# Kernel tuning notes

Measured on AMD Instinct MI355X. Metric: run time of the kernel, lower is better.

Reference implementation:

```python
import jax, jax.numpy as jnp
import numpy as np

D_MODEL = 1024
D_INNER = 2048  # d_model * expand_factor
EPS = 1e-6


def setup_inputs() -> dict:
    key = jax.random.key(0)
    ks = jax.random.split(key, 9)
    s_in = 1.0 / np.sqrt(D_MODEL)
    s_out = 1.0 / np.sqrt(D_INNER)
    x = jax.random.normal(ks[0], (4, 2048, D_MODEL), dtype=jnp.float32)
    # weights stored as [in, out] (transpose of nn.Linear layout)
    Wq = jax.random.uniform(ks[1], (D_MODEL, D_INNER), jnp.float32, -s_in, s_in)
    bq = jax.random.uniform(ks[2], (D_INNER,), jnp.float32, -s_in, s_in)
    Wk = jax.random.uniform(ks[3], (D_MODEL, D_INNER), jnp.float32, -s_in, s_in)
    bk = jax.random.uniform(ks[4], (D_INNER,), jnp.float32, -s_in, s_in)
    Wv = jax.random.uniform(ks[5], (D_MODEL, D_INNER), jnp.float32, -s_in, s_in)
    bv = jax.random.uniform(ks[6], (D_INNER,), jnp.float32, -s_in, s_in)
    Wo = jax.random.uniform(ks[7], (D_INNER, D_MODEL), jnp.float32, -s_out, s_out)
    bo = jax.random.uniform(ks[8], (D_MODEL,), jnp.float32, -s_out, s_out)
    return {"x": x, "Wq": Wq, "bq": bq, "Wk": Wk, "bk": bk,
            "Wv": Wv, "bv": bv, "Wo": Wo, "bo": bo}


def _phi(x):
    """ELU + 1 feature map (positive features)."""
    return jax.nn.elu(x) + 1.0


def reference(x, Wq, bq, Wk, bk, Wv, bv, Wo, bo):
    # x: [B, N, d_model]
    Q = _phi(x @ Wq + bq)          # [B, N, d_inner]
    K = _phi(x @ Wk + bk)          # [B, N, d_inner]
    V = x @ Wv + bv                # [B, N, d_inner]
    n = x.shape[1]
    # Causal linear attention; identical math to cumsum-of-outer-products:
    # numerator_n = sum_{m<=n} (Q_n . K_m) V_m ; denominator_n = sum_{m<=n} Q_n . K_m
    scores = jnp.einsum("bnd,bmd->bnm", Q, K)            # [B, N, N]
    mask = jnp.tril(jnp.ones((n, n), dtype=scores.dtype))
    scores = scores * mask
    numerator = jnp.einsum("bnm,bme->bne", scores, V)    # [B, N, d_inner]
    denominator = scores.sum(axis=-1, keepdims=True) + EPS
    out = numerator / denominator
    return out @ Wo + bo           # [B, N, d_model] (dropout is identity in eval)
```

## Files before the change

### kernel.cpp

```cpp
#include <hip/hip_runtime.h>
#include <hip/hip_bf16.h>


#define D_MODEL 1024
#define D_INNER 2048
#define SEQ     2048
#define NBATCH  4
#define MTOT    (NBATCH * SEQ)

typedef __attribute__((ext_vector_type(8))) __bf16 bf16x8;
typedef __attribute__((ext_vector_type(4))) float  f32x4;
typedef __attribute__((ext_vector_type(8))) short  short8v;
typedef __attribute__((ext_vector_type(4))) int    int4v;
typedef __attribute__((ext_vector_type(8))) int    int8v;

__device__ __forceinline__ short f2bf(float f) {
  union { float f; unsigned u; } x; x.f = f;
  unsigned r = x.u + 0x7fffu + ((x.u >> 16) & 1u);
  return (short)(r >> 16);
}
__device__ __forceinline__ float bf2f(short s) {
  union { unsigned u; float f; } x; x.u = ((unsigned)(unsigned short)s) << 16;
  return x.f;
}

__device__ __forceinline__ unsigned char f2fp8(float f) {
  union { float f; unsigned u; } x; x.f = f;
  const unsigned s = (x.u >> 24) & 0x80u;
  const unsigned a = x.u & 0x7fffffffu;
  if (a >= 0x43E00000u) return (unsigned char)(s | 0x7Eu);
  if (a < 0x3C800000u) {
    union { float f; unsigned u; } y; y.u = a;
    const int mi = (int)rintf(y.f * 512.0f);
    return (unsigned char)(s | (unsigned)mi);
  }
  const unsigned r = a + 0x7FFFFu + ((a >> 20) & 1u);
  const unsigned E = (r >> 23) - 120u;
  return (unsigned char)(s | (E << 3) | ((r >> 20) & 7u));
}

typedef const void __attribute__((address_space(1)))* as1cv;
typedef void __attribute__((address_space(3)))* as3v;

__device__ __forceinline__ void gload_lds16(const void* g, void* l) {
  __builtin_amdgcn_global_load_lds((as1cv)g, (as3v)l, 16, 0, 0);
}

__device__ __forceinline__ f32x4 mfma16(bf16x8 a, bf16x8 b, f32x4 c) {
  return __builtin_amdgcn_mfma_f32_16x16x32_bf16(a, b, c, 0, 0, 0);
}

__device__ __forceinline__ f32x4 mfma_fp8(int8v a, int8v b, f32x4 c) {
  asm("v_mfma_f32_16x16x128_f8f6f4 %0, %1, %2, %0"
      : "+v"(c) : "v"(a), "v"(b));
  return c;
}

__device__ __forceinline__ void gemm_pipe(const short* __restrict__ A, int lda, int aRowBase,
                                          const short* __restrict__ B, int ldb, int bRowBase,
                                          int k0, int k1, short* smem, f32x4 acc[4][4]) {
  const int t    = threadIdx.x;
  const int lane = t & 63, wid = t >> 6;
  const int wr = wid >> 1, wc = wid & 1;
  const int lrow = lane & 15, kblk = lane >> 4;

  const int r0 = t >> 2;
  const int sc = ((t & 3) ^ ((t >> 3) & 3)) * 8;
  const short* pA = A + (size_t)(aRowBase + r0) * lda + (k0 + sc);
  const short* pB = B + (size_t)(bRowBase + r0) * ldb + (k0 + sc);
  const size_t rA = (size_t)64 * lda;
  const size_t rB = (size_t)64 * ldb;

  int aoff[4], boff[4];
#pragma unroll
  for (int m = 0; m < 4; ++m) {
    const int row = wr * 64 + m * 16 + lrow;
    aoff[m] = (row * 64 + kblk * 16) ^ (((row >> 1) & 3) << 4);
  }
#pragma unroll
  for (int n = 0; n < 4; ++n) {
    const int row = wc * 64 + n * 16 + lrow;
    boff[n] = (row * 64 + kblk * 16) ^ (((row >> 1) & 3) << 4);
  }
  const char* cs = (const char*)smem;

#define STG(bufShorts) do {                                                    \
    gload_lds16(pA, smem + (bufShorts) + t * 8);                               \
    gload_lds16(pA + rA, smem + (bufShorts) + 2048 + t * 8);                   \
    gload_lds16(pB, smem + (bufShorts) + 4096 + t * 8);                        \
    gload_lds16(pB + rB, smem + (bufShorts) + 6144 + t * 8);                   \
    pA += 32; pB += 32;                                                        \
  } while (0)

#define CSTEP(bufBytes) do {                                                   \
    bf16x8 a[4], b[4];                                                         \
    _Pragma("unroll") for (int m = 0; m < 4; ++m)                              \
      a[m] = *(const bf16x8*)(cs + (bufBytes) + aoff[m]);                      \
    _Pragma("unroll") for (int n = 0; n < 4; ++n)                              \
      b[n] = *(const bf16x8*)(cs + (bufBytes) + 8192 + boff[n]);               \
    _Pragma("unroll") for (int m = 0; m < 4; ++m)                              \
      _Pragma("unroll") for (int n = 0; n < 4; ++n)                            \
        acc[m][n] = mfma16(a[m], b[n], acc[m][n]);                             \
  } while (0)

  STG(0);
  __syncthreads();
  for (int k = k0; k < k1; k += 64) {
    if (k + 32 < k1) STG(8192);
    CSTEP(0);
    __syncthreads();
    if (k + 64 < k1) STG(0);
    CSTEP(16384);
    __syncthreads();
  }
#undef STG
#undef CSTEP
}

__device__ __forceinline__ void gemm_pipe8(const unsigned char* __restrict__ A, int lda, int aRowBase,
                                           const unsigned char* __restrict__ B, int ldb, int bRowBase,
                                           int k0, int k1, char* smem, f32x4 acc[4][4]) {
  const int t    = threadIdx.x;
  const int lane = t & 63, wid = t >> 6;
  const int wr = wid >> 1, wc = wid & 1;
  const int lrow = lane & 15, kblk = lane >> 4;

  const int srow = t >> 3;
  const int scol = (((t & 7) ^ ((t >> 3) & 7)) << 4);
  const unsigned char* pA = A + (size_t)(aRowBase + srow) * lda + (k0 + scol);
  const unsigned char* pB = B + (size_t)(bRowBase + srow) * ldb + (k0 + scol);

  int aoff[4][2], boff[4][2];
#pragma unroll
  for (int m = 0; m < 4; ++m) {
    const int row = wr * 64 + m * 16 + lrow;
#pragma unroll
    for (int j = 0; j < 2; ++j)
      aoff[m][j] = row * 128 + (((kblk * 2 + j) ^ (row & 7)) << 4);
  }
#pragma unroll
  for (int n = 0; n < 4; ++n) {
    const int row = wc * 64 + n * 16 + lrow;
#pragma unroll
    for (int j = 0; j < 2; ++j)
      boff[n][j] = row * 128 + (((kblk * 2 + j) ^ (row & 7)) << 4);
  }

#define STG8(bufB) do {                                                        \
    _Pragma("unroll") for (int i = 0; i < 4; ++i) {                            \
      gload_lds16(pA + (size_t)(32 * i) * lda, smem + (bufB) + i * 4096 + t * 16);      \
      gload_lds16(pB + (size_t)(32 * i) * ldb, smem + (bufB) + 16384 + i * 4096 + t * 16); \
    }                                                                          \
    pA += 128; pB += 128;                                                      \
  } while (0)

#define CSTEP8(bufB) do {                                                      \
    int8v a[4], b[4];                                                          \
    _Pragma("unroll") for (int m = 0; m < 4; ++m)                              \
      _Pragma("unroll") for (int j = 0; j < 2; ++j)                            \
        ((int4v*)&a[m])[j] = *(const int4v*)(smem + (bufB) + aoff[m][j]);      \
    _Pragma("unroll") for (int n = 0; n < 4; ++n)                              \
      _Pragma("unroll") for (int j = 0; j < 2; ++j)                            \
        ((int4v*)&b[n])[j] = *(const int4v*)(smem + (bufB) + 16384 + boff[n][j]); \
    _Pragma("unroll") for (int m = 0; m < 4; ++m)                              \
      _Pragma("unroll") for (int n = 0; n < 4; ++n)                            \
        acc[m][n] = mfma_fp8(a[m], b[n], acc[m][n]);                           \
  } while (0)

  STG8(0);
  __syncthreads();
  for (int k = k0; k < k1; k += 256) {
    if (k + 128 < k1) STG8(32768);
    CSTEP8(0);
    __syncthreads();
    if (k + 256 < k1) STG8(0);
    CSTEP8(32768);
    __syncthreads();
  }
#undef STG8
#undef CSTEP8
}

#define GEMM_PRE                                           \
  __shared__ __align__(16) short smem[4 * 4096];           \
  f32x4 acc[4][4];                                         \
  _Pragma("unroll")                                        \
  for (int m = 0; m < 4; ++m)                              \
    _Pragma("unroll")                                      \
    for (int n = 0; n < 4; ++n) acc[m][n] = (f32x4){0.f, 0.f, 0.f, 0.f};

#define GEMM_PRE8                                          \
  __shared__ __align__(16) char smem8[65536];              \
  f32x4 acc[4][4];                                         \
  _Pragma("unroll")                                        \
  for (int m = 0; m < 4; ++m)                              \
    _Pragma("unroll")                                      \
    for (int n = 0; n < 4; ++n) acc[m][n] = (f32x4){0.f, 0.f, 0.f, 0.f};

#define EPILOG_VARS                                        \
  const int lane = threadIdx.x & 63;                       \
  const int wid  = threadIdx.x >> 6;                       \
  const int wr = wid >> 1, wc = wid & 1;                   \
  const int lrow = lane & 15, kblk = lane >> 4;

__global__ __launch_bounds__(256) void k_proj_qk8(const unsigned char* __restrict__ X8,
                                                  const unsigned char* __restrict__ WT8,
                                                  const float* __restrict__ bq,
                                                  const float* __restrict__ bk,
                                                  unsigned char* __restrict__ Qm8,
                                                  unsigned char* __restrict__ Km8) {
  GEMM_PRE8
  const int blockM = blockIdx.y * 128;
  const int blockN = blockIdx.x * 128;
  gemm_pipe8(X8, D_MODEL, blockM, WT8, D_MODEL, blockN, 0, D_MODEL, smem8, acc);
  EPILOG_VARS
  const int seg = blockN >> 11;
  const float* bias = (seg == 0) ? bq : bk;
  unsigned char* dst = (seg == 0) ? Qm8 : Km8;
#pragma unroll
  for (int m = 0; m < 4; ++m)
#pragma unroll
    for (int n = 0; n < 4; ++n) {
      const int e = (blockN & 2047) + wc * 64 + n * 16 + lrow;
      const float bvv = bias[e];
#pragma unroll
      for (int j = 0; j < 4; ++j) {
        const int row = blockM + wr * 64 + m * 16 + kblk * 4 + j;
        float v = acc[m][n][j] + bvv;
        v = (v > 0.f) ? (v + 1.f) : __expf(v);
        dst[(size_t)row * D_INNER + e] = f2fp8(v);
      }
    }
}

__global__ __launch_bounds__(256) void k_proj_v(const short* __restrict__ X,
                                                const short* __restrict__ WvT,
                                                const float* __restrict__ bv,
                                                short* __restrict__ vT) {
  GEMM_PRE
  const int blockM = blockIdx.y * 128;
  const int blockN = blockIdx.x * 128;
  gemm_pipe(X, D_MODEL, blockM, WvT, D_MODEL, blockN, 0, D_MODEL, smem, acc);
  EPILOG_VARS
#pragma unroll
  for (int m = 0; m < 4; ++m)
#pragma unroll
    for (int n = 0; n < 4; ++n) {
      const int cl = wc * 64 + n * 16 + lrow;
      const float bvv = bv[blockN + cl];
#pragma unroll
      for (int j = 0; j < 4; ++j) {
        const int rl = wr * 64 + m * 16 + kblk * 4 + j;
        int byte = cl * 256 + rl * 2;
        byte ^= (cl & 7) << 5;
        *(short*)((char*)smem + byte) = f2bf(acc[m][n][j] + bvv);
      }
    }
  __syncthreads();
  const int b   = blockM >> 11;
  const int mm0 = blockM & 2047;
  const int er  = threadIdx.x >> 1;
  const int hf  = threadIdx.x & 1;
  short* dst = vT + ((size_t)b * D_INNER + blockN + er) * SEQ + mm0 + hf * 64;
#pragma unroll
  for (int i = 0; i < 8; ++i) {
    int byte = er * 256 + hf * 128 + i * 16;
    byte ^= (er & 7) << 5;
    ((short8v*)dst)[i] = *(const short8v*)((const char*)smem + byte);
  }
}

__global__ __launch_bounds__(256) void k_qkt8(const unsigned char* __restrict__ Q8,
                                              const unsigned char* __restrict__ K8,
                                              short* __restrict__ S,
                                              float* __restrict__ den_part) {
  const int b = blockIdx.y;
  const int t = blockIdx.x;
  int ib = (int)((-1.0f + sqrtf(8.0f * (float)t + 1.0f)) * 0.5f);
  while ((ib + 1) * (ib + 2) / 2 <= t) ++ib;
  while (ib * (ib + 1) / 2 > t) --ib;
  const int jb = t - ib * (ib + 1) / 2;
  GEMM_PRE8
  short* Sb = S + (size_t)b * SEQ * SEQ;
  gemm_pipe8(Q8 + (size_t)b * SEQ * D_INNER, D_INNER, ib * 128,
             K8 + (size_t)b * SEQ * D_INNER, D_INNER, jb * 128,
             0, D_INNER, smem8, acc);
  EPILOG_VARS
  const bool diag = (jb == ib);
  float sums[4][4];
#pragma unroll
  for (int m = 0; m < 4; ++m)
#pragma unroll
    for (int j = 0; j < 4; ++j) sums[m][j] = 0.f;
#pragma unroll
  for (int m = 0; m < 4; ++m)
#pragma unroll
    for (int n = 0; n < 4; ++n) {
      const int col = jb * 128 + wc * 64 + n * 16 + lrow;
#pragma unroll
      for (int j = 0; j < 4; ++j) {
        const int row = ib * 128 + wr * 64 + m * 16 + kblk * 4 + j;
        float v = acc[m][n][j];
        if (diag && col > row) v = 0.f;
        const short bs = f2bf(v);
        Sb[(size_t)row * SEQ + col] = bs;
        sums[m][j] += bf2f(bs);
      }
    }
#pragma unroll
  for (int m = 0; m < 4; ++m)
#pragma unroll
    for (int j = 0; j < 4; ++j) {
      float red = sums[m][j];
      red += __shfl_xor(red, 1, 64);
      red += __shfl_xor(red, 2, 64);
      red += __shfl_xor(red, 4, 64);
      red += __shfl_xor(red, 8, 64);
      if (lrow == 0) {
        const int rloc = wr * 64 + m * 16 + kblk * 4 + j;
        den_part[(size_t)(2 * jb + wc) * MTOT + b * SEQ + ib * 128 + rloc] = red;
      }
    }
}

__global__ __launch_bounds__(256) void k_av(const short* __restrict__ S,
                                            const short* __restrict__ VT,
                                            const float* __restrict__ den_part,
                                            short* __restrict__ attn) {
  const int b = blockIdx.z;
  const int ib = 15 - blockIdx.y;
  const int eb = blockIdx.x;
  __shared__ float dnm[128];
  {
    const int t = threadIdx.x;
    if (t < 128) {
      float s = 1e-6f;
      const int nv = 2 * (ib + 1);
      const float* dp = den_part + b * SEQ + ib * 128 + t;
      for (int q = 0; q < nv; ++q) s += dp[(size_t)q * MTOT];
      dnm[t] = 1.0f / s;
    }
  }
  GEMM_PRE
  gemm_pipe(S + (size_t)b * SEQ * SEQ, SEQ, ib * 128,
            VT + (size_t)b * (size_t)D_INNER * SEQ, SEQ, eb * 128,
            0, (ib + 1) * 128, smem, acc);
  EPILOG_VARS
  const int blockM = ib * 128;
#pragma unroll
  for (int m = 0; m < 4; ++m)
#pragma unroll
    for (int j = 0; j < 4; ++j) {
      const int rloc = wr * 64 + m * 16 + kblk * 4 + j;
      const int row = blockM + rloc;
      const float rcp = dnm[rloc];
#pragma unroll
      for (int n = 0; n < 4; ++n) {
        const int col = eb * 128 + wc * 64 + n * 16 + lrow;
        attn[((size_t)(b * SEQ + row)) * D_INNER + col] = f2bf(acc[m][n][j] * rcp);
      }
    }
}

__global__ __launch_bounds__(256) void k_out(const short* __restrict__ A,
                                             const short* __restrict__ WoT,
                                             const float* __restrict__ bo,
                                             float* __restrict__ out) {
  GEMM_PRE
  const int blockM = blockIdx.y * 128;
  const int blockN = blockIdx.x * 128;
  gemm_pipe(A, D_INNER, blockM, WoT, D_INNER, blockN, 0, D_INNER, smem, acc);
  EPILOG_VARS
#pragma unroll
  for (int m = 0; m < 4; ++m)
#pragma unroll
    for (int n = 0; n < 4; ++n) {
      const int col = blockN + wc * 64 + n * 16 + lrow;
      const float bvv = bo[col];
#pragma unroll
      for (int j = 0; j < 4; ++j) {
        const int row = blockM + wr * 64 + m * 16 + kblk * 4 + j;
        out[(size_t)row * D_MODEL + col] = acc[m][n][j] + bvv;
      }
    }
}

__global__ void k_cvt(const float* __restrict__ in, short* __restrict__ outb,
                      unsigned char* __restrict__ out8, int n4) {
  int i = blockIdx.x * blockDim.x + threadIdx.x;
  const int stride = gridDim.x * blockDim.x;
  for (; i < n4; i += stride) {
    float4 v = ((const float4*)in)[i];
    short4 o;
    o.x = f2bf(v.x); o.y = f2bf(v.y); o.z = f2bf(v.z); o.w = f2bf(v.w);
    ((short4*)outb)[i] = o;
    uchar4 q;
    q.x = f2fp8(v.x); q.y = f2fp8(v.y); q.z = f2fp8(v.z); q.w = f2fp8(v.w);
    ((uchar4*)out8)[i] = q;
  }
}

__global__ __launch_bounds__(256) void k_transposeAll(const float* __restrict__ w0,
                                                      const float* __restrict__ w1,
                                                      const float* __restrict__ w2,
                                                      const float* __restrict__ w3,
                                                      unsigned char* __restrict__ wqkT8,
                                                      short* __restrict__ wvT,
                                                      short* __restrict__ woT) {
  __shared__ float tl[32][33];
  const int z = blockIdx.z;
  const float* in = (z == 0) ? w0 : (z == 1) ? w1 : (z == 2) ? w2 : w3;
  const int R = (z < 3) ? 1024 : 2048;
  const int C = (z < 3) ? 2048 : 1024;
  const int nbx = C >> 5;
  const int c0 = (blockIdx.x % nbx) * 32, r0 = (blockIdx.x / nbx) * 32;
  const int tx = threadIdx.x & 31, ty = (threadIdx.x >> 5) * 4;
#pragma unroll
  for (int i = 0; i < 4; ++i)
    tl[ty + i][tx] = in[(size_t)(r0 + ty + i) * C + (c0 + tx)];
  __syncthreads();
  if (z < 2) {
    unsigned char* o = wqkT8 + (size_t)z * D_INNER * D_MODEL;
#pragma unroll
    for (int i = 0; i < 4; ++i)
      o[(size_t)(c0 + ty + i) * R + (r0 + tx)] = f2fp8(tl[tx][ty + i]);
  } else {
    short* o = (z == 2) ? wvT : woT;
#pragma unroll
    for (int i = 0; i < 4; ++i)
      o[(size_t)(c0 + ty + i) * R + (r0 + tx)] = f2bf(tl[tx][ty + i]);
  }
}

extern "C" void kernel_launch(void* const* d_in, const int* in_sizes, int n_in,
                              void* d_out, int out_size, void* d_ws, size_t ws_size,
                              hipStream_t stream) {
  const float* x  = (const float*)d_in[0];
  const float* Wq = (const float*)d_in[1];
  const float* bq = (const float*)d_in[2];
  const float* Wk = (const float*)d_in[3];
  const float* bk = (const float*)d_in[4];
  const float* Wv = (const float*)d_in[5];
  const float* bv = (const float*)d_in[6];
  const float* Wo = (const float*)d_in[7];
  const float* bo = (const float*)d_in[8];
  float* out = (float*)d_out;

  short* xb    = (short*)d_ws;
  short* wvT   = xb    + (size_t)MTOT * D_MODEL;
  short* woT   = wvT   + (size_t)D_INNER * D_MODEL;
  short* vT    = woT   + (size_t)D_MODEL * D_INNER;
  short* Sc    = vT    + (size_t)MTOT * D_INNER;
  short* attn  = Sc    + (size_t)NBATCH * SEQ * SEQ;
  unsigned char* x8    = (unsigned char*)(attn + (size_t)MTOT * D_INNER);
  unsigned char* wqkT8 = x8    + (size_t)MTOT * D_MODEL;
  unsigned char* Qm8   = wqkT8 + (size_t)2 * D_INNER * D_MODEL;
  unsigned char* Km8   = Qm8   + (size_t)MTOT * D_INNER;
  float* den_part      = (float*)(Km8 + (size_t)MTOT * D_INNER);

  dim3 b256(256);
  k_cvt<<<2048, b256, 0, stream>>>(x, xb, x8, MTOT * D_MODEL / 4);
  k_transposeAll<<<dim3(2048, 1, 4), b256, 0, stream>>>(Wq, Wk, Wv, Wo, wqkT8, wvT, woT);

  k_proj_qk8<<<dim3(32, 64), b256, 0, stream>>>(x8, wqkT8, bq, bk, Qm8, Km8);
  k_proj_v  <<<dim3(16, 64), b256, 0, stream>>>(xb, wvT, bv, vT);

  k_qkt8<<<dim3(136, NBATCH), b256, 0, stream>>>(Qm8, Km8, Sc, den_part);
  k_av  <<<dim3(16, 16, NBATCH), b256, 0, stream>>>(Sc, vT, den_part, attn);
  k_out <<<dim3(8, 64), b256, 0, stream>>>(attn, woT, bo, out);
}
```

Measured before the change: 303.8 us.

## Reassociate attention output as S·(V·Wo) to shrink the causal GEMM width

Computes V·Wo first into a per-batch transposed buffer, then multiplies the causal score matrix by this narrower product and applies the normalization and output bias in the epilogue. This halves the N dimension of the triangular score-value GEMM and removes the separate attention-output intermediate and final projection kernel. The trade-off is an extra rounding to bf16 of V·Wo before the causal sum, which may change numerical error.

Result: faster. 284.5 us (-6.3%).

```diff
diff --git a/kernel.cpp b/kernel.cpp
--- a/kernel.cpp
+++ b/kernel.cpp
@@ -236,7 +236,7 @@
 __global__ __launch_bounds__(256) void k_proj_v(const short* __restrict__ X,
                                                 const short* __restrict__ WvT,
                                                 const float* __restrict__ bv,
-                                                short* __restrict__ vT) {
+                                                short* __restrict__ V) {
   GEMM_PRE
   const int blockM = blockIdx.y * 128;
   const int blockN = blockIdx.x * 128;
@@ -246,14 +246,35 @@
   for (int m = 0; m < 4; ++m)
 #pragma unroll
     for (int n = 0; n < 4; ++n) {
+      const int e = blockN + wc * 64 + n * 16 + lrow;
+      const float bvv = bv[e];
+#pragma unroll
+      for (int j = 0; j < 4; ++j) {
+        const int row = blockM + wr * 64 + m * 16 + kblk * 4 + j;
+        V[(size_t)row * D_INNER + e] = f2bf(acc[m][n][j] + bvv);
+      }
+    }
+}
+
+__global__ __launch_bounds__(256) void k_vw(const short* __restrict__ V,
+                                            const short* __restrict__ WoT,
+                                            short* __restrict__ w2T) {
+  GEMM_PRE
+  const int blockM = blockIdx.y * 128;
+  const int blockN = blockIdx.x * 128;
+  gemm_pipe(V, D_INNER, blockM, WoT, D_INNER, blockN, 0, D_INNER, smem, acc);
+  EPILOG_VARS
+#pragma unroll
+  for (int m = 0; m < 4; ++m)
+#pragma unroll
+    for (int n = 0; n < 4; ++n) {
       const int cl = wc * 64 + n * 16 + lrow;
-      const float bvv = bv[blockN + cl];
 #pragma unroll
       for (int j = 0; j < 4; ++j) {
         const int rl = wr * 64 + m * 16 + kblk * 4 + j;
         int byte = cl * 256 + rl * 2;
         byte ^= (cl & 7) << 5;
-        *(short*)((char*)smem + byte) = f2bf(acc[m][n][j] + bvv);
+        *(short*)((char*)smem + byte) = f2bf(acc[m][n][j]);
       }
     }
   __syncthreads();
@@ -261,7 +282,7 @@
   const int mm0 = blockM & 2047;
   const int er  = threadIdx.x >> 1;
   const int hf  = threadIdx.x & 1;
-  short* dst = vT + ((size_t)b * D_INNER + blockN + er) * SEQ + mm0 + hf * 64;
+  short* dst = w2T + ((size_t)b * D_MODEL + blockN + er) * SEQ + mm0 + hf * 64;
 #pragma unroll
   for (int i = 0; i < 8; ++i) {
     int byte = er * 256 + hf * 128 + i * 16;
@@ -323,10 +344,11 @@
     }
 }
 
-__global__ __launch_bounds__(256) void k_av(const short* __restrict__ S,
-                                            const short* __restrict__ VT,
+__global__ __launch_bounds__(256) void k_sv(const short* __restrict__ S,
+                                            const short* __restrict__ W2T,
                                             const float* __restrict__ den_part,
-                                            short* __restrict__ attn) {
+                                            const float* __restrict__ bo,
+                                            float* __restrict__ out) {
   const int b = blockIdx.z;
   const int ib = 15 - blockIdx.y;
   const int eb = blockIdx.x;
@@ -343,7 +365,7 @@
   }
   GEMM_PRE
   gemm_pipe(S + (size_t)b * SEQ * SEQ, SEQ, ib * 128,
-            VT + (size_t)b * (size_t)D_INNER * SEQ, SEQ, eb * 128,
+            W2T + (size_t)b * (size_t)D_MODEL * SEQ, SEQ, eb * 128,
             0, (ib + 1) * 128, smem, acc);
   EPILOG_VARS
   const int blockM = ib * 128;
@@ -357,30 +379,7 @@
 #pragma unroll
       for (int n = 0; n < 4; ++n) {
         const int col = eb * 128 + wc * 64 + n * 16 + lrow;
-        attn[((size_t)(b * SEQ + row)) * D_INNER + col] = f2bf(acc[m][n][j] * rcp);
-      }
-    }
-}
-
-__global__ __launch_bounds__(256) void k_out(const short* __restrict__ A,
-                                             const short* __restrict__ WoT,
-                                             const float* __restrict__ bo,
-                                             float* __restrict__ out) {
-  GEMM_PRE
-  const int blockM = blockIdx.y * 128;
-  const int blockN = blockIdx.x * 128;
-  gemm_pipe(A, D_INNER, blockM, WoT, D_INNER, blockN, 0, D_INNER, smem, acc);
-  EPILOG_VARS
-#pragma unroll
-  for (int m = 0; m < 4; ++m)
-#pragma unroll
-    for (int n = 0; n < 4; ++n) {
-      const int col = blockN + wc * 64 + n * 16 + lrow;
-      const float bvv = bo[col];
-#pragma unroll
-      for (int j = 0; j < 4; ++j) {
-        const int row = blockM + wr * 64 + m * 16 + kblk * 4 + j;
-        out[(size_t)row * D_MODEL + col] = acc[m][n][j] + bvv;
+        out[((size_t)(b * SEQ + row)) * D_MODEL + col] = acc[m][n][j] * rcp + bo[col];
       }
     }
 }
@@ -449,10 +448,10 @@
   short* xb    = (short*)d_ws;
   short* wvT   = xb    + (size_t)MTOT * D_MODEL;
   short* woT   = wvT   + (size_t)D_INNER * D_MODEL;
-  short* vT    = woT   + (size_t)D_MODEL * D_INNER;
-  short* Sc    = vT    + (size_t)MTOT * D_INNER;
-  short* attn  = Sc    + (size_t)NBATCH * SEQ * SEQ;
-  unsigned char* x8    = (unsigned char*)(attn + (size_t)MTOT * D_INNER);
+  short* V     = woT   + (size_t)D_MODEL * D_INNER;
+  short* Sc    = V     + (size_t)MTOT * D_INNER;
+  short* w2T   = Sc    + (size_t)NBATCH * SEQ * SEQ;
+  unsigned char* x8    = (unsigned char*)(w2T + (size_t)NBATCH * D_MODEL * SEQ);
   unsigned char* wqkT8 = x8    + (size_t)MTOT * D_MODEL;
   unsigned char* Qm8   = wqkT8 + (size_t)2 * D_INNER * D_MODEL;
   unsigned char* Km8   = Qm8   + (size_t)MTOT * D_INNER;
@@ -463,9 +462,9 @@
   k_transposeAll<<<dim3(2048, 1, 4), b256, 0, stream>>>(Wq, Wk, Wv, Wo, wqkT8, wvT, woT);
 
   k_proj_qk8<<<dim3(32, 64), b256, 0, stream>>>(x8, wqkT8, bq, bk, Qm8, Km8);
-  k_proj_v  <<<dim3(16, 64), b256, 0, stream>>>(xb, wvT, bv, vT);
+  k_proj_v  <<<dim3(16, 64), b256, 0, stream>>>(xb, wvT, bv, V);
 
   k_qkt8<<<dim3(136, NBATCH), b256, 0, stream>>>(Qm8, Km8, Sc, den_part);
-  k_av  <<<dim3(16, 16, NBATCH), b256, 0, stream>>>(Sc, vT, den_part, attn);
-  k_out <<<dim3(8, 64), b256, 0, stream>>>(attn, woT, bo, out);
-}
+  k_vw  <<<dim3(8, 64), b256, 0, stream>>>(V, woT, w2T);
+  k_sv  <<<dim3(8, 16, NBATCH), b256, 0, stream>>>(Sc, w2T, den_part, bo, out);
+}
```
